# Kernel tuning notes

Hardware: AMD Instinct MI355X
Metric: run time of the kernel (lower is better)

Reference implementation:

```python
import jax, jax.numpy as jnp
import numpy as np

D_MODEL = 2048
D_STATE = 128
D_CONV = 4
NHEADS = 64
NGROUPS = 1
HEAD_DIM = 64
CHUNK = 128
EPS = 1e-5
D_INNER = NHEADS * HEAD_DIM                       # 4096
CONV_DIM = D_INNER + 2 * NGROUPS * D_STATE        # 4352
D_IN_PROJ = 2 * D_INNER + 2 * NGROUPS * D_STATE + NHEADS  # 8512


def setup_inputs() -> dict:
    key = jax.random.key(0)
    ks = jax.random.split(key, 9)
    B, S = 2, 4096
    return dict(
        hidden_states=jax.random.normal(ks[0], (B, S, D_MODEL), jnp.float32),
        W_in=jax.random.normal(ks[1], (D_MODEL, D_IN_PROJ), jnp.float32) * 0.02,
        conv_w=jax.random.normal(ks[2], (CONV_DIM, D_CONV), jnp.float32) * 0.2,
        conv_b=jax.random.normal(ks[3], (CONV_DIM,), jnp.float32) * 0.1,
        # A must be negative (stable SSM): A = -exp(u), u ~ U[0,2)
        A=-jnp.exp(jax.random.uniform(ks[4], (NHEADS,), jnp.float32, 0.0, 2.0)),
        D=jax.random.normal(ks[5], (NHEADS,), jnp.float32),
        dt_bias=jax.random.normal(ks[6], (NHEADS,), jnp.float32),
        norm_w=jnp.ones((D_INNER,), jnp.float32),
        W_out=jax.random.normal(ks[7], (D_INNER, D_MODEL), jnp.float32) * 0.02,
    )


def _silu(x):
    return x * jax.nn.sigmoid(x)


def _causal_conv1d(x, w, b):
    # depthwise causal conv with silu; x [B,S,C], w [C,K], b [C]
    K = w.shape[1]
    S = x.shape[1]
    xp = jnp.pad(x, ((0, 0), (K - 1, 0), (0, 0)))
    y = sum(xp[:, k:k + S, :] * w[None, None, :, k].swapaxes(-1, -1) for k in range(0))
    y = jnp.zeros_like(x)
    for k in range(K):
        y = y + xp[:, k:k + S, :] * w[:, k][None, None, :]
    return _silu(y + b)


def _ssd(x, dt, A, Bm, Cm, chunk):
    # Mamba2 chunked SSD scan.
    # x [b,s,h,p]; dt [b,s,h] (>0); A [h]; Bm,Cm [b,s,g,n]
    b, s, h, p = x.shape
    g, n = Bm.shape[2], Bm.shape[3]
    hh = h // g
    c = s // chunk
    x = x.reshape(b, c, chunk, g, hh, p)
    dt = dt.reshape(b, c, chunk, g, hh)
    Bm = Bm.reshape(b, c, chunk, g, n)
    Cm = Cm.reshape(b, c, chunk, g, n)
    dA = dt * A.reshape(g, hh)                 # [b,c,l,g,hh]
    dA_cs = jnp.cumsum(dA, axis=2)             # [b,c,l,g,hh]
    dtx = dt[..., None] * x                    # [b,c,l,g,hh,p]
    # intra-chunk (diagonal blocks): L[i,j] = exp(sum_{j<k<=i} dA)
    diff = dA_cs[:, :, :, None] - dA_cs[:, :, None, :]   # [b,c,i,j,g,hh]
    mask = jnp.tril(jnp.ones((chunk, chunk), bool))
    L = jnp.exp(jnp.where(mask[None, None, :, :, None, None], diff, -jnp.inf))
    Y = jnp.einsum('bcign,bcjgn,bcijgh,bcjghp->bcighp', Cm, Bm, L, dtx)
    # chunk-final states
    decay = jnp.exp(dA_cs[:, :, -1:] - dA_cs)            # [b,c,l,g,hh]
    states = jnp.einsum('bcjgn,bcjgh,bcjghp->bcghpn', Bm, decay, dtx)
    chunk_decay = jnp.exp(dA_cs[:, :, -1])               # [b,c,g,hh]
    def step(prev, inp):
        cd, st = inp
        return cd[..., None, None] * prev + st, prev
    init = jnp.zeros_like(states[:, 0])
    _, prevs = jax.lax.scan(step, init,
                            (jnp.moveaxis(chunk_decay, 1, 0), jnp.moveaxis(states, 1, 0)))
    prevs = jnp.moveaxis(prevs, 0, 1)                    # [b,c,g,hh,p,n] state entering each chunk
    Y = Y + jnp.einsum('bcign,bcghpn,bcigh->bcighp', Cm, prevs, jnp.exp(dA_cs))
    return Y.reshape(b, s, h, p)


def reference(hidden_states, W_in, conv_w, conv_b, A, D, dt_bias, norm_w, W_out):
    Bsz, S, _ = hidden_states.shape
    zxbcdt = hidden_states @ W_in                        # [B,S,d_in_proj]
    z = zxbcdt[..., :D_INNER]
    xbc = zxbcdt[..., D_INNER:D_INNER + CONV_DIM]
    dt = zxbcdt[..., D_INNER + CONV_DIM:]                # [B,S,nheads]
    xbc = _causal_conv1d(xbc, conv_w, conv_b)            # silu-activated causal conv
    x = xbc[..., :D_INNER].reshape(Bsz, S, NHEADS, HEAD_DIM)
    Bm = xbc[..., D_INNER:D_INNER + NGROUPS * D_STATE].reshape(Bsz, S, NGROUPS, D_STATE)
    Cm = xbc[..., D_INNER + NGROUPS * D_STATE:].reshape(Bsz, S, NGROUPS, D_STATE)
    dt = jax.nn.softplus(dt + dt_bias)                   # delta_softplus, dt_limit=(0,inf)
    y = _ssd(x, dt, A, Bm, Cm, CHUNK)
    y = y + D[None, None, :, None] * x                   # skip (D) term
    y = y.reshape(Bsz, S, D_INNER)
    # gated RMSNorm (norm_before_gate=False): normalize(y * silu(z)), grouped
    yg = y * _silu(z)
    gsz = D_INNER // NGROUPS
    ygr = yg.reshape(Bsz, S, NGROUPS, gsz)
    rms = jax.lax.rsqrt(jnp.mean(ygr * ygr, axis=-1, keepdims=True) + EPS)
    yn = (ygr * rms).reshape(Bsz, S, D_INNER) * norm_w
    return yn @ W_out
```

## Files before the change

### kernel.cpp

```cpp
#include <hip/hip_runtime.h>
#include <hip/hip_bf16.h>

typedef __bf16 bf16_t;
typedef bf16_t bf16x8 __attribute__((ext_vector_type(8)));
typedef float f32x4 __attribute__((ext_vector_type(4)));

#define TOK 8192
#define DMODEL 2048
#define DINNER 4096
#define XBCN 4352
#define DSTATE 128
#define NH 64
#define HD 64
#define NBC 64
#define WINT_ROWS 8448

__device__ __forceinline__ void gld16(const bf16_t* g, bf16_t* l) {
  __builtin_amdgcn_global_load_lds((const __attribute__((address_space(1))) void*)g,
                                   (__attribute__((address_space(3))) void*)l, 16, 0, 0);
}

__device__ __forceinline__ f32x4 mfma16(bf16x8 a, bf16x8 b, f32x4 c) {
  return __builtin_amdgcn_mfma_f32_16x16x32_bf16(a, b, c, 0, 0, 0);
}

__device__ __forceinline__ bf16x8 ldsr(unsigned addr) {
  f32x4 r;
  asm volatile("ds_read_b128 %0, %1" : "=v"(r) : "v"(addr));
  return __builtin_bit_cast(bf16x8, r);
}


__global__ __launch_bounds__(256)
void cast_split_kernel(const float* __restrict__ in, bf16_t* __restrict__ hi,
                       bf16_t* __restrict__ lo, size_t n) {
  size_t i = ((size_t)blockIdx.x * 256 + threadIdx.x) * 8;
  if (i + 8 > n) return;
  float4 a = *(const float4*)(in + i);
  float4 b = *(const float4*)(in + i + 4);
  float v[8] = {a.x,a.y,a.z,a.w,b.x,b.y,b.z,b.w};
  bf16x8 h, l;
#pragma unroll
  for (int j = 0; j < 8; ++j) {
    h[j] = (bf16_t)v[j];
    l[j] = (bf16_t)(v[j] - (float)h[j]);
  }
  *(bf16x8*)(hi + i) = h;
  *(bf16x8*)(lo + i) = l;
}

__global__ __launch_bounds__(256)
void transpose_cast_kernel(const float* __restrict__ in, bf16_t* __restrict__ out,
                           int R, int C, int outRows) {
  __shared__ float tile[32][33];
  const int c0 = blockIdx.x * 32;
  const int r0 = blockIdx.y * 32;
  const int tx = threadIdx.x & 31;
  const int ty = threadIdx.x >> 5;
#pragma unroll
  for (int k = 0; k < 4; ++k) {
    int r = r0 + ty + k*8;
    int c = c0 + tx;
    tile[ty + k*8][tx] = (c < C) ? in[(size_t)r * C + c] : 0.f;
  }
  __syncthreads();
#pragma unroll
  for (int k = 0; k < 4; ++k) {
    int oc = c0 + ty + k*8;
    int orr = r0 + tx;
    out[(size_t)oc * R + orr] = (bf16_t)tile[tx][ty + k*8];
  }
}

__global__ __launch_bounds__(256)
void wdt_split_kernel(const float* __restrict__ Win, bf16_t* __restrict__ Whi,
                      bf16_t* __restrict__ Wlo) {
  const int h = threadIdx.x & 63;
  const int k0 = blockIdx.x * 256 + (threadIdx.x >> 6) * 64;
#pragma unroll 4
  for (int i = 0; i < 64; ++i) {
    int k = k0 + i;
    float v = Win[(size_t)k * 8512 + 8448 + h];
    bf16_t hv = (bf16_t)v;
    Whi[(size_t)h * DMODEL + k] = hv;
    Wlo[(size_t)h * DMODEL + k] = (bf16_t)(v - (float)hv);
  }
}

template <typename OutT>
__global__ __launch_bounds__(512, 2)
void gemm256(const bf16_t* __restrict__ A, const bf16_t* __restrict__ B,
             OutT* __restrict__ C0, OutT* __restrict__ C1,
             long M, long N, long K, long splitN, int gridX) {
  __shared__ bf16_t sA[2][2][8192];
  __shared__ bf16_t sB[2][2][8192];
  const int tid = threadIdx.x;
  const int lane = tid & 63;
  const int wid = tid >> 6;
  const int wr = wid >> 2;
  const int wc = wid & 3;

  const int x = blockIdx.x & 7;
  const int q = blockIdx.x >> 3;
  const long bm = (long)(x * 4 + (q & 3)) * 256;
  const long bn = (long)(q >> 2) * 256;

  const int srow = (wid >> 1) * 16 + (lane & 15);
  const int skof = (wid & 1) * 32 + (lane >> 4) * 8;
  const bf16_t* Abase = A + (bm + srow) * K + skof;
  const bf16_t* Bbase = B + (bn + srow) * K + skof;

  auto stageA = [&](int buf, int h, long kt) {
    const bf16_t* s = Abase + (long)h * 128 * K + kt;
    gld16(s,          &sA[buf][h][wid * 512]);
    gld16(s + 64 * K, &sA[buf][h][4096 + wid * 512]);
  };
  auto stageB = [&](int buf, int h, long kt) {
    const bf16_t* s = Bbase + (long)h * 128 * K + kt;
    gld16(s,          &sB[buf][h][wid * 512]);
    gld16(s + 64 * K, &sB[buf][h][4096 + wid * 512]);
  };

  const unsigned sAb = (unsigned)(uintptr_t)(__attribute__((address_space(3))) void*)&sA[0][0][0]
                       + (unsigned)lane * 16 + (unsigned)wr * 8192;
  const unsigned sBb = (unsigned)(uintptr_t)(__attribute__((address_space(3))) void*)&sB[0][0][0]
                       + (unsigned)lane * 16 + (unsigned)wc * 4096;

  stageA(0, 0, 0); stageB(0, 0, 0); stageB(0, 1, 0); stageA(0, 1, 0);

  f32x4 acc[8][4] = {};
  bf16x8 a0[4][2], a1[4][2], b0[2][2], b1[2][2];
  int cur = 0;
  const int NT = (int)(K >> 6);

  for (int t = 0; t < NT; ++t) {
    const bool fin = (t == NT - 1);
    const long ktn = (long)(t + 1) * 64;
    const unsigned ab = sAb + (unsigned)cur * 32768;
    const unsigned bb = sBb + (unsigned)cur * 32768;

    asm volatile("s_waitcnt vmcnt(0)\n\ts_barrier" ::: "memory");

#pragma unroll
    for (int mi = 0; mi < 4; ++mi) {
      a0[mi][0] = ldsr(ab + (mi*2+0)*1024);
      a0[mi][1] = ldsr(ab + (mi*2+1)*1024);
    }
#pragma unroll
    for (int ni = 0; ni < 2; ++ni) {
      b0[ni][0] = ldsr(bb + (ni*2+0)*1024);
      b0[ni][1] = ldsr(bb + (ni*2+1)*1024);
    }
    if (!fin) { stageA(cur ^ 1, 0, ktn); stageB(cur ^ 1, 0, ktn); }
    asm volatile("s_waitcnt lgkmcnt(0)" ::: "memory");
    __builtin_amdgcn_sched_barrier(0);

#pragma unroll
    for (int ni = 0; ni < 2; ++ni) {
      b1[ni][0] = ldsr(bb + 16384 + (ni*2+0)*1024);
      b1[ni][1] = ldsr(bb + 16384 + (ni*2+1)*1024);
    }
    if (!fin) stageB(cur ^ 1, 1, ktn);
    __builtin_amdgcn_sched_barrier(0);
    __builtin_amdgcn_s_setprio(1);
#pragma unroll
    for (int mi = 0; mi < 4; ++mi)
#pragma unroll
      for (int ni = 0; ni < 2; ++ni) {
        acc[mi][ni] = mfma16(a0[mi][0], b0[ni][0], acc[mi][ni]);
        acc[mi][ni] = mfma16(a0[mi][1], b0[ni][1], acc[mi][ni]);
      }
    __builtin_amdgcn_s_setprio(0);
    __builtin_amdgcn_sched_barrier(0);
    asm volatile("s_waitcnt lgkmcnt(0)" ::: "memory");
    __builtin_amdgcn_sched_barrier(0);

#pragma unroll
    for (int mi = 0; mi < 4; ++mi) {
      a1[mi][0] = ldsr(ab + 16384 + (mi*2+0)*1024);
      a1[mi][1] = ldsr(ab + 16384 + (mi*2+1)*1024);
    }
    if (!fin) stageA(cur ^ 1, 1, ktn);
    __builtin_amdgcn_sched_barrier(0);
    __builtin_amdgcn_s_setprio(1);
#pragma unroll
    for (int mi = 0; mi < 4; ++mi)
#pragma unroll
      for (int ni = 0; ni < 2; ++ni) {
        acc[mi][2 + ni] = mfma16(a0[mi][0], b1[ni][0], acc[mi][2 + ni]);
        acc[mi][2 + ni] = mfma16(a0[mi][1], b1[ni][1], acc[mi][2 + ni]);
      }
    __builtin_amdgcn_s_setprio(0);
    __builtin_amdgcn_sched_barrier(0);
    asm volatile("s_waitcnt lgkmcnt(0)" ::: "memory");
    __builtin_amdgcn_sched_barrier(0);

    __builtin_amdgcn_s_setprio(1);
#pragma unroll
    for (int mi = 0; mi < 4; ++mi)
#pragma unroll
      for (int ni = 0; ni < 2; ++ni) {
        acc[4 + mi][2 + ni] = mfma16(a1[mi][0], b1[ni][0], acc[4 + mi][2 + ni]);
        acc[4 + mi][2 + ni] = mfma16(a1[mi][1], b1[ni][1], acc[4 + mi][2 + ni]);
      }
#pragma unroll
    for (int mi = 0; mi < 4; ++mi)
#pragma unroll
      for (int ni = 0; ni < 2; ++ni) {
        acc[4 + mi][ni] = mfma16(a1[mi][0], b0[ni][0], acc[4 + mi][ni]);
        acc[4 + mi][ni] = mfma16(a1[mi][1], b0[ni][1], acc[4 + mi][ni]);
      }
    __builtin_amdgcn_s_setprio(0);
    __builtin_amdgcn_sched_barrier(0);
    cur ^= 1;
  }

  const int cr = (lane >> 4) * 4;
  const int cc = lane & 15;
  OutT* Cb;
  long col0, ldc;
  if (bn < splitN) { Cb = C0; col0 = bn; ldc = splitN; }
  else             { Cb = C1; col0 = bn - splitN; ldc = N - splitN; }
#pragma unroll
  for (int mi = 0; mi < 8; ++mi) {
    long row = bm + (mi >> 2) * 128 + wr * 64 + (mi & 3) * 16 + cr;
#pragma unroll
    for (int ni = 0; ni < 4; ++ni) {
      long col = col0 + (ni >> 1) * 128 + wc * 32 + (ni & 1) * 16 + cc;
      OutT* p = Cb + row * ldc + col;
#pragma unroll
      for (int r = 0; r < 4; ++r) p[(long)r * ldc] = (OutT)acc[mi][ni][r];
    }
  }
}

__global__ __launch_bounds__(256)
void dt_mfma_kernel(const bf16_t* __restrict__ Ahi, const bf16_t* __restrict__ Alo,
                    const bf16_t* __restrict__ Whi, const bf16_t* __restrict__ Wlo,
                    float* __restrict__ dtraw) {
  __shared__ bf16_t sAh[4096], sAl[4096], sBh[2048], sBl[2048];
  const int tid = threadIdx.x;
  const int lane = tid & 63;
  const int w = tid >> 6;
  const long bm = (long)blockIdx.x * 128;
  const int rlo = lane & 15;
  const int kq = lane >> 4;

  const bf16_t* Ah0 = Ahi + (bm + 2*w*16 + rlo) * (long)DMODEL + kq*8;
  const bf16_t* Ah1 = Ah0 + 16*(long)DMODEL;
  const bf16_t* Al0 = Alo + (bm + 2*w*16 + rlo) * (long)DMODEL + kq*8;
  const bf16_t* Al1 = Al0 + 16*(long)DMODEL;
  const bf16_t* Bh0 = Whi + (w*16 + rlo) * (long)DMODEL + kq*8;
  const bf16_t* Bl0 = Wlo + (w*16 + rlo) * (long)DMODEL + kq*8;

  f32x4 acc[2][4] = {};

  for (int kt = 0; kt < DMODEL; kt += 32) {
    __syncthreads();
    gld16(Ah0 + kt, &sAh[(2*w)*512]);
    gld16(Ah1 + kt, &sAh[(2*w+1)*512]);
    gld16(Al0 + kt, &sAl[(2*w)*512]);
    gld16(Al1 + kt, &sAl[(2*w+1)*512]);
    gld16(Bh0 + kt, &sBh[w*512]);
    gld16(Bl0 + kt, &sBl[w*512]);
    __syncthreads();
    bf16x8 ah[2], al[2], bh[4], bl[4];
#pragma unroll
    for (int i = 0; i < 2; ++i) {
      ah[i] = *(const bf16x8*)&sAh[((2*w + i)*64 + lane)*8];
      al[i] = *(const bf16x8*)&sAl[((2*w + i)*64 + lane)*8];
    }
#pragma unroll
    for (int n = 0; n < 4; ++n) {
      bh[n] = *(const bf16x8*)&sBh[(n*64 + lane)*8];
      bl[n] = *(const bf16x8*)&sBl[(n*64 + lane)*8];
    }
#pragma unroll
    for (int mi = 0; mi < 2; ++mi)
#pragma unroll
      for (int n = 0; n < 4; ++n) {
        acc[mi][n] = mfma16(ah[mi], bh[n], acc[mi][n]);
        acc[mi][n] = mfma16(ah[mi], bl[n], acc[mi][n]);
        acc[mi][n] = mfma16(al[mi], bh[n], acc[mi][n]);
      }
  }

  const int cr = (lane >> 4) * 4;
  const int cc = lane & 15;
#pragma unroll
  for (int mi = 0; mi < 2; ++mi)
#pragma unroll
    for (int n = 0; n < 4; ++n)
#pragma unroll
      for (int r = 0; r < 4; ++r)
        dtraw[(bm + 2*w*16 + mi*16 + cr + r) * 64 + n*16 + cc] = acc[mi][n][r];
}

__global__ __launch_bounds__(256)
void conv_kernel(const bf16_t* __restrict__ xbc, const float* __restrict__ cw,
                 const float* __restrict__ cb, bf16_t* __restrict__ xo,
                 bf16_t* __restrict__ Bout, bf16_t* __restrict__ Cout) {
  const int c = blockIdx.x * 256 + threadIdx.x;
  const int t0 = blockIdx.y * 8;
  const int bstart = (t0 >> 12) << 12;
  const float w0 = cw[c*4+0], w1 = cw[c*4+1], w2 = cw[c*4+2], w3 = cw[c*4+3];
  const float bias = cb[c];
  float in[11];
#pragma unroll
  for (int k = 0; k < 11; ++k) {
    int t = t0 - 3 + k;
    in[k] = (t >= bstart) ? (float)xbc[(size_t)t * XBCN + c] : 0.f;
  }
#pragma unroll
  for (int i = 0; i < 8; ++i) {
    float v = bias + w0*in[i] + w1*in[i+1] + w2*in[i+2] + w3*in[i+3];
    float s = v / (1.f + __expf(-v));
    int t = t0 + i;
    bf16_t o = (bf16_t)s;
    if (c < DINNER)           xo[(size_t)t * DINNER + c] = o;
    else if (c < DINNER+128)  Bout[(size_t)t * DSTATE + (c - DINNER)] = o;
    else                      Cout[(size_t)t * DSTATE + (c - DINNER - 128)] = o;
  }
}

__global__ __launch_bounds__(256)
void dt_scan_kernel(const float* __restrict__ dtraw, const float* __restrict__ dt_bias,
                    const float* __restrict__ Avec, float* __restrict__ dt_s,
                    float* __restrict__ dAcs, float* __restrict__ cdec) {
  const int wid = blockIdx.x * 4 + (threadIdx.x >> 6);
  const int lane = threadIdx.x & 63;
  const int h = wid & 63;
  const int bc = wid >> 6;
  const long tok0 = (long)bc * 128;
  const float Ah = Avec[h];
  const float bias = dt_bias[h];
  float v0 = dtraw[(tok0 + lane)*64 + h] + bias;
  float v1 = dtraw[(tok0 + 64 + lane)*64 + h] + bias;
  float d0 = (v0 > 20.f) ? v0 : log1pf(expf(v0));
  float d1 = (v1 > 20.f) ? v1 : log1pf(expf(v1));
  float s0 = d0 * Ah;
  float s1 = d1 * Ah;
#pragma unroll
  for (int off = 1; off < 64; off <<= 1) {
    float t = __shfl_up(s0, off);
    if (lane >= off) s0 += t;
  }
  float tot0 = __shfl(s0, 63);
#pragma unroll
  for (int off = 1; off < 64; off <<= 1) {
    float t = __shfl_up(s1, off);
    if (lane >= off) s1 += t;
  }
  s1 += tot0;
  const size_t base = (size_t)wid * 128;
  dt_s[base + lane] = d0;
  dt_s[base + 64 + lane] = d1;
  dAcs[base + lane] = s0;
  dAcs[base + 64 + lane] = s1;
  if (lane == 63) cdec[wid] = __expf(s1);
}

__global__ __launch_bounds__(256)
void states_kernel(const bf16_t* __restrict__ x, const bf16_t* __restrict__ Bm,
                   const float* __restrict__ dt_s, const float* __restrict__ dAcs,
                   bf16_t* __restrict__ states) {
  __shared__ bf16_t sDtx[8192];
  __shared__ bf16_t sBd[16384];
  __shared__ float sDt[128];
  __shared__ float sDec[128];
  const int wid = blockIdx.x;
  const int h = wid & 63;
  const int bc = wid >> 6;
  const int tid = threadIdx.x;
  const int lane = tid & 63;
  const int w = tid >> 6;
  const long tok0 = (long)bc * 128;
  const size_t dbase = (size_t)wid * 128;

  if (tid < 128) {
    sDt[tid] = dt_s[dbase + tid];
  } else {
    int j = tid - 128;
    sDec[j] = __expf(dAcs[dbase + 127] - dAcs[dbase + j]);
  }
  __syncthreads();

  {
    const int jj0 = tid >> 3;
    const int pg = (tid & 7) * 8;
#pragma unroll
    for (int t = 0; t < 4; ++t) {
      int j = t*32 + jj0;
      bf16x8 xv = *(const bf16x8*)&x[(tok0 + j)*(long)DINNER + h*64 + pg];
      float dtj = sDt[j];
      int kq = (j >> 5) * 4;
      int qe = ((j >> 3) & 3) * 16;
      int e = j & 7;
#pragma unroll
      for (int i = 0; i < 8; ++i) {
        int p = pg + i;
        sDtx[((kq + (p>>4))*64 + qe + (p&15))*8 + e] = (bf16_t)((float)xv[i]*dtj);
      }
    }
    const int jj1 = tid >> 4;
    const int ng = (tid & 15) * 8;
#pragma unroll
    for (int t = 0; t < 8; ++t) {
      int j = t*16 + jj1;
      bf16x8 bv = *(const bf16x8*)&Bm[(tok0 + j)*(long)DSTATE + ng];
      float dec = sDec[j];
      int kq = (j >> 5) * 8;
      int qe = ((j >> 3) & 3) * 16;
      int e = j & 7;
#pragma unroll
      for (int i = 0; i < 8; ++i) {
        int n = ng + i;
        sBd[((kq + (n>>4))*64 + qe + (n&15))*8 + e] = (bf16_t)((float)bv[i]*dec);
      }
    }
  }
  __syncthreads();

  f32x4 acc[4][2] = {};
#pragma unroll
  for (int kt = 0; kt < 4; ++kt) {
    bf16x8 aF[4], bF[2];
#pragma unroll
    for (int mt = 0; mt < 4; ++mt) aF[mt] = *(const bf16x8*)&sDtx[((kt*4 + mt)*64 + lane)*8];
#pragma unroll
    for (int nt = 0; nt < 2; ++nt) bF[nt] = *(const bf16x8*)&sBd[((kt*8 + w*2 + nt)*64 + lane)*8];
#pragma unroll
    for (int mt = 0; mt < 4; ++mt)
#pragma unroll
      for (int nt = 0; nt < 2; ++nt)
        acc[mt][nt] = mfma16(aF[mt], bF[nt], acc[mt][nt]);
  }

  bf16_t* S = states + (size_t)wid * (HD * DSTATE);
  const int cr = (lane >> 4) * 4;
  const int cc = lane & 15;
#pragma unroll
  for (int mt = 0; mt < 4; ++mt)
#pragma unroll
    for (int nt = 0; nt < 2; ++nt) {
      int n = (w*2 + nt)*16 + cc;
#pragma unroll
      for (int r = 0; r < 4; ++r) {
        int p = mt*16 + cr + r;
        S[(size_t)p*DSTATE + n] = (bf16_t)acc[mt][nt][r];
      }
    }
}

__global__ __launch_bounds__(256)
void scan_kernel(bf16_t* __restrict__ sp, const float* __restrict__ cdec) {
  const size_t gid = (size_t)blockIdx.x * 256 + threadIdx.x;
  const int n = gid & 127;
  const int p = (gid >> 7) & 63;
  const int h = (gid >> 13) & 63;
  const int b = (int)(gid >> 19);
  float prev = 0.f;
  const size_t pn = (size_t)p * 128 + n;
  for (int c = 0; c < 32; ++c) {
    const int wid = (b*32 + c)*64 + h;
    const size_t idx = (size_t)wid * 8192 + pn;
    float s = (float)sp[idx];
    sp[idx] = (bf16_t)prev;
    prev = cdec[wid] * prev + s;
  }
}

__global__ __launch_bounds__(256)
void ssd_y_kernel(bf16_t* __restrict__ xy, const bf16_t* __restrict__ Bm,
                  const bf16_t* __restrict__ Cm, const bf16_t* __restrict__ prevs,
                  const float* __restrict__ dt_s, const float* __restrict__ dAcs,
                  const float* __restrict__ Dvec) {
  __shared__ bf16_t sG[16384];
  __shared__ bf16_t sDtx[8192];
  __shared__ float sDA[128];
  __shared__ float sEA[128];
  __shared__ float sDt[128];

  const int wid = blockIdx.x;
  const int h = wid & 63;
  const int bc = wid >> 6;
  const int tid = threadIdx.x;
  const int lane = tid & 63;
  const int w = tid >> 6;
  const long tok0 = (long)bc * 128;
  const size_t dbase = (size_t)wid * 128;

  if (tid < 128) {
    float v = dAcs[dbase + tid];
    sDA[tid] = v;
    sEA[tid] = __expf(v);
  } else {
    sDt[tid - 128] = dt_s[dbase + tid - 128];
  }
  __syncthreads();

  {
    const int jj0 = tid >> 3;
    const int pg = (tid & 7) * 8;
#pragma unroll
    for (int t = 0; t < 4; ++t) {
      int j = t*32 + jj0;
      bf16x8 xv = *(const bf16x8*)&xy[(tok0 + j)*(long)DINNER + h*64 + pg];
      float dtj = sDt[j];
      int kq = (j >> 5) * 4;
      int qe = ((j >> 3) & 3) * 16;
      int e = j & 7;
#pragma unroll
      for (int i = 0; i < 8; ++i) {
        int p = pg + i;
        sDtx[((kq + (p>>4))*64 + qe + (p&15))*8 + e] = (bf16_t)((float)xv[i]*dtj);
      }
    }
  }

  const int arow = (w*2)*16 + (lane & 15);
  const int koff = (lane >> 4) * 8;
  bf16x8 aCm[2][4];
#pragma unroll
  for (int mi = 0; mi < 2; ++mi)
#pragma unroll
    for (int kt = 0; kt < 4; ++kt)
      aCm[mi][kt] = *(const bf16x8*)&Cm[(tok0 + arow + mi*16)*(long)DSTATE + kt*32 + koff];

  const bf16_t* P = prevs + (size_t)wid * 8192;
  f32x4 accY[2][4] = {};
#pragma unroll
  for (int kt = 0; kt < 4; ++kt) {
    bf16x8 bP[4];
#pragma unroll
    for (int ni = 0; ni < 4; ++ni)
      bP[ni] = *(const bf16x8*)&P[(size_t)(ni*16 + (lane & 15))*DSTATE + kt*32 + koff];
#pragma unroll
    for (int mi = 0; mi < 2; ++mi)
#pragma unroll
      for (int ni = 0; ni < 4; ++ni)
        accY[mi][ni] = mfma16(aCm[mi][kt], bP[ni], accY[mi][ni]);
  }
  const int cr = (lane >> 4) * 4;
  const int cc = lane & 15;
#pragma unroll
  for (int mi = 0; mi < 2; ++mi)
#pragma unroll
    for (int r = 0; r < 4; ++r) {
      float e = sEA[(w*2 + mi)*16 + cr + r];
#pragma unroll
      for (int ni = 0; ni < 4; ++ni) accY[mi][ni][r] *= e;
    }

  f32x4 accS[2][8] = {};
#pragma unroll
  for (int kt = 0; kt < 4; ++kt) {
    bf16x8 bB[8];
#pragma unroll
    for (int nt = 0; nt < 8; ++nt)
      bB[nt] = *(const bf16x8*)&Bm[(tok0 + nt*16 + (lane & 15))*(long)DSTATE + kt*32 + koff];
#pragma unroll
    for (int mi = 0; mi < 2; ++mi)
#pragma unroll
      for (int nt = 0; nt < 8; ++nt)
        accS[mi][nt] = mfma16(aCm[mi][kt], bB[nt], accS[mi][nt]);
  }

#pragma unroll
  for (int mi = 0; mi < 2; ++mi)
#pragma unroll
    for (int nt = 0; nt < 8; ++nt)
#pragma unroll
      for (int r = 0; r < 4; ++r) {
        int i = (w*2 + mi)*16 + cr + r;
        int j = nt*16 + cc;
        float g = (i >= j) ? accS[mi][nt][r] * __expf(sDA[i] - sDA[j]) : 0.f;
        sG[(((j>>5)*8 + (i>>4))*64 + ((j>>3)&3)*16 + (i&15))*8 + (j&7)] = (bf16_t)g;
      }
  __syncthreads();

#pragma unroll
  for (int kt = 0; kt < 4; ++kt) {
    bf16x8 aG[2], bD[4];
#pragma unroll
    for (int mi = 0; mi < 2; ++mi) aG[mi] = *(const bf16x8*)&sG[((kt*8 + w*2 + mi)*64 + lane)*8];
#pragma unroll
    for (int ni = 0; ni < 4; ++ni) bD[ni] = *(const bf16x8*)&sDtx[((kt*4 + ni)*64 + lane)*8];
#pragma unroll
    for (int mi = 0; mi < 2; ++mi)
#pragma unroll
      for (int ni = 0; ni < 4; ++ni)
        accY[mi][ni] = mfma16(aG[mi], bD[ni], accY[mi][ni]);
  }

  const float Dh = Dvec[h];
#pragma unroll
  for (int mi = 0; mi < 2; ++mi)
#pragma unroll
    for (int ni = 0; ni < 4; ++ni)
#pragma unroll
      for (int r = 0; r < 4; ++r) {
        long tokr = tok0 + (w*2 + mi)*16 + cr + r;
        int p = ni*16 + cc;
        long idx = tokr * DINNER + h*64 + p;
        float xv = (float)xy[idx];
        xy[idx] = (bf16_t)(accY[mi][ni][r] + Dh * xv);
      }
}

__global__ __launch_bounds__(256)
void gate_kernel(const bf16_t* __restrict__ y, const bf16_t* __restrict__ z,
                 const float* __restrict__ norm_w, bf16_t* __restrict__ yn) {
  const int tok = blockIdx.x;
  const int tid = threadIdx.x;
  const int lane = tid & 63;
  const int w = tid >> 6;
  const bf16_t* yrow = y + (size_t)tok * DINNER;
  const bf16_t* zrow = z + (size_t)tok * DINNER;
  float local[16];
  float ss = 0.f;
#pragma unroll
  for (int v = 0; v < 2; ++v) {
    int col = tid*16 + v*8;
    bf16x8 yv = *(const bf16x8*)&yrow[col];
    bf16x8 zv = *(const bf16x8*)&zrow[col];
#pragma unroll
    for (int i = 0; i < 8; ++i) {
      float zf = (float)zv[i];
      float g = zf / (1.f + __expf(-zf));
      float t = (float)yv[i] * g;
      local[v*8 + i] = t;
      ss += t*t;
    }
  }
#pragma unroll
  for (int off = 32; off > 0; off >>= 1) ss += __shfl_xor(ss, off);
  __shared__ float red[4];
  if (lane == 0) red[w] = ss;
  __syncthreads();
  float rms = rsqrtf((red[0]+red[1]+red[2]+red[3]) * (1.f/DINNER) + 1e-5f);
  bf16_t* orow = yn + (size_t)tok * DINNER;
#pragma unroll
  for (int v = 0; v < 2; ++v) {
    int col = tid*16 + v*8;
    bf16x8 o;
#pragma unroll
    for (int i = 0; i < 8; ++i) o[i] = (bf16_t)(local[v*8+i] * rms * norm_w[col+i]);
    *(bf16x8*)&orow[col] = o;
  }
}

extern "C" void kernel_launch(void* const* d_in, const int* in_sizes, int n_in,
                              void* d_out, int out_size, void* d_ws, size_t ws_size,
                              hipStream_t stream) {
  const float* hidden  = (const float*)d_in[0];
  const float* W_in    = (const float*)d_in[1];
  const float* conv_w  = (const float*)d_in[2];
  const float* conv_b  = (const float*)d_in[3];
  const float* Avec    = (const float*)d_in[4];
  const float* Dvec    = (const float*)d_in[5];
  const float* dt_bias = (const float*)d_in[6];
  const float* norm_w  = (const float*)d_in[7];
  const float* W_out   = (const float*)d_in[8];

  char* ws = (char*)d_ws;
  size_t off = 0;
  auto take = [&](size_t bytes) -> char* {
    char* p = ws + off;
    off += (bytes + 255) & ~(size_t)255;
    return p;
  };
  bf16_t* R1    = (bf16_t*)take((size_t)NBC * NH * HD * DSTATE * 2);
  bf16_t* WinT  = (bf16_t*)take((size_t)WINT_ROWS * DMODEL * 2);
  bf16_t* xbc   = (bf16_t*)take((size_t)TOK * XBCN * 2);
  bf16_t* xconv = (bf16_t*)take((size_t)TOK * DINNER * 2);
  bf16_t* Bmat  = (bf16_t*)take((size_t)TOK * DSTATE * 2);
  bf16_t* Cmat  = (bf16_t*)take((size_t)TOK * DSTATE * 2);
  float*  dtraw = (float*)take((size_t)TOK * NH * 4);
  float*  dt_s  = (float*)take((size_t)TOK * NH * 4);
  float*  dAcs  = (float*)take((size_t)TOK * NH * 4);
  float*  cdec  = (float*)take((size_t)NBC * NH * 4);
  bf16_t* Wdth  = (bf16_t*)take((size_t)NH * DMODEL * 2);
  bf16_t* Wdtl  = (bf16_t*)take((size_t)NH * DMODEL * 2);
  if (off > ws_size) return;

  bf16_t* Xb      = R1;
  bf16_t* Xlo     = xbc;
  bf16_t* statesB = R1;
  bf16_t* ynbuf   = R1;
  bf16_t* WoutT   = WinT;
  bf16_t* zbuf    = (bf16_t*)d_out;
  float*  out     = (float*)d_out;

  cast_split_kernel<<<(TOK*DMODEL)/2048, 256, 0, stream>>>(hidden, Xb, Xlo, (size_t)TOK*DMODEL);
  wdt_split_kernel<<<DMODEL/256, 256, 0, stream>>>(W_in, Wdth, Wdtl);
  dt_mfma_kernel<<<TOK/128, 256, 0, stream>>>(Xb, Xlo, Wdth, Wdtl, dtraw);
  transpose_cast_kernel<<<dim3(WINT_ROWS/32, DMODEL/32), 256, 0, stream>>>(W_in, WinT, DMODEL, 8512, WINT_ROWS);
  gemm256<bf16_t><<<(TOK/256)*(WINT_ROWS/256), 512, 0, stream>>>(
      Xb, WinT, zbuf, xbc, TOK, WINT_ROWS, DMODEL, DINNER, WINT_ROWS/256);
  transpose_cast_kernel<<<dim3(DMODEL/32, DINNER/32), 256, 0, stream>>>(W_out, WoutT, DINNER, DMODEL, DMODEL);
  conv_kernel<<<dim3(XBCN/256, TOK/8), 256, 0, stream>>>(xbc, conv_w, conv_b, xconv, Bmat, Cmat);
  dt_scan_kernel<<<(NBC*NH)/4, 256, 0, stream>>>(dtraw, dt_bias, Avec, dt_s, dAcs, cdec);
  states_kernel<<<NBC*NH, 256, 0, stream>>>(xconv, Bmat, dt_s, dAcs, statesB);
  scan_kernel<<<(NBC*NH*HD*DSTATE)/(32*256), 256, 0, stream>>>(statesB, cdec);
  ssd_y_kernel<<<NBC*NH, 256, 0, stream>>>(xconv, Bmat, Cmat, statesB, dt_s, dAcs, Dvec);
  gate_kernel<<<TOK, 256, 0, stream>>>(xconv, zbuf, norm_w, ynbuf);
  gemm256<float><<<(TOK/256)*(DMODEL/256), 512, 0, stream>>>(
      ynbuf, WoutT, out, out, TOK, DMODEL, DINNER, DMODEL, DMODEL/256);
}
```

Before: 1.053 ms.

## Restructure GEMM main loop into 8-phase ping-pong pipeline with partial vmcnt waits

Rewrites the 256x256 bf16 GEMM k-loop to process two k-tiles per iteration in eight phases. Each phase issues LDS reads and one quarter-tile global-to-LDS prefetch, then runs an MFMA quadrant between barriers. It prefetches deeper, with the next buffer staged up front, and waits on vmcnt(6) instead of vmcnt(0), so global loads stay in flight across the MFMA phases. The cost is more s_barrier calls per tile and tighter ordering assumptions on buffer reuse, which could cause races if a stage overwrites data still being read.

```diff
diff --git a/kernel.cpp b/kernel.cpp
--- a/kernel.cpp
+++ b/kernel.cpp
@@ -86,6 +86,51 @@
     Wlo[(size_t)h * DMODEL + k] = (bf16_t)(v - (float)hv);
   }
 }
+
+#define PH_MID() \
+  __builtin_amdgcn_sched_barrier(0); \
+  asm volatile("s_barrier" ::: "memory"); \
+  asm volatile("s_waitcnt lgkmcnt(0)" ::: "memory"); \
+  __builtin_amdgcn_sched_barrier(0); \
+  __builtin_amdgcn_s_setprio(1)
+
+#define PH_END() \
+  __builtin_amdgcn_s_setprio(0); \
+  __builtin_amdgcn_sched_barrier(0); \
+  asm volatile("s_barrier" ::: "memory")
+
+#define PH_END_VM6() \
+  __builtin_amdgcn_s_setprio(0); \
+  __builtin_amdgcn_sched_barrier(0); \
+  asm volatile("s_waitcnt vmcnt(6)\n\ts_barrier" ::: "memory")
+
+#define PH_END_VM0() \
+  __builtin_amdgcn_s_setprio(0); \
+  __builtin_amdgcn_sched_barrier(0); \
+  asm volatile("s_waitcnt vmcnt(0)\n\ts_barrier" ::: "memory")
+
+#define RD_A(arr, base) \
+  _Pragma("unroll") \
+  for (int mi = 0; mi < 4; ++mi) { \
+    arr[mi][0] = ldsr((base) + (mi*2+0)*1024); \
+    arr[mi][1] = ldsr((base) + (mi*2+1)*1024); \
+  }
+
+#define RD_B(arr, base) \
+  _Pragma("unroll") \
+  for (int ni = 0; ni < 2; ++ni) { \
+    arr[ni][0] = ldsr((base) + (ni*2+0)*1024); \
+    arr[ni][1] = ldsr((base) + (ni*2+1)*1024); \
+  }
+
+#define MMAQ(MB, NB, aa, bb2) \
+  _Pragma("unroll") \
+  for (int mi = 0; mi < 4; ++mi) \
+    _Pragma("unroll") \
+    for (int ni = 0; ni < 2; ++ni) { \
+      acc[(MB)+mi][(NB)+ni] = mfma16(aa[mi][0], bb2[ni][0], acc[(MB)+mi][(NB)+ni]); \
+      acc[(MB)+mi][(NB)+ni] = mfma16(aa[mi][1], bb2[ni][1], acc[(MB)+mi][(NB)+ni]); \
+    }
 
 template <typename OutT>
 __global__ __launch_bounds__(512, 2)
@@ -121,98 +166,81 @@
     gld16(s + 64 * K, &sB[buf][h][4096 + wid * 512]);
   };
 
-  const unsigned sAb = (unsigned)(uintptr_t)(__attribute__((address_space(3))) void*)&sA[0][0][0]
-                       + (unsigned)lane * 16 + (unsigned)wr * 8192;
-  const unsigned sBb = (unsigned)(uintptr_t)(__attribute__((address_space(3))) void*)&sB[0][0][0]
-                       + (unsigned)lane * 16 + (unsigned)wc * 4096;
+  const unsigned ldsA = (unsigned)(uintptr_t)(__attribute__((address_space(3))) void*)&sA[0][0][0]
+                        + (unsigned)lane * 16 + (unsigned)wr * 8192;
+  const unsigned ldsB = (unsigned)(uintptr_t)(__attribute__((address_space(3))) void*)&sB[0][0][0]
+                        + (unsigned)lane * 16 + (unsigned)wc * 4096;
+  const unsigned ab0 = ldsA;
+  const unsigned ab0h = ldsA + 16384;
+  const unsigned ab1 = ldsA + 32768;
+  const unsigned ab1h = ldsA + 49152;
+  const unsigned bb0 = ldsB;
+  const unsigned bb0h = ldsB + 16384;
+  const unsigned bb1 = ldsB + 32768;
+  const unsigned bb1h = ldsB + 49152;
 
   stageA(0, 0, 0); stageB(0, 0, 0); stageB(0, 1, 0); stageA(0, 1, 0);
+  stageA(1, 0, 64); stageB(1, 0, 64); stageB(1, 1, 64);
+  __builtin_amdgcn_sched_barrier(0);
+  asm volatile("s_waitcnt vmcnt(6)\n\ts_barrier" ::: "memory");
 
   f32x4 acc[8][4] = {};
   bf16x8 a0[4][2], a1[4][2], b0[2][2], b1[2][2];
-  int cur = 0;
-  const int NT = (int)(K >> 6);
-
-  for (int t = 0; t < NT; ++t) {
-    const bool fin = (t == NT - 1);
-    const long ktn = (long)(t + 1) * 64;
-    const unsigned ab = sAb + (unsigned)cur * 32768;
-    const unsigned bb = sBb + (unsigned)cur * 32768;
-
-    asm volatile("s_waitcnt vmcnt(0)\n\ts_barrier" ::: "memory");
-
-#pragma unroll
-    for (int mi = 0; mi < 4; ++mi) {
-      a0[mi][0] = ldsr(ab + (mi*2+0)*1024);
-      a0[mi][1] = ldsr(ab + (mi*2+1)*1024);
-    }
-#pragma unroll
-    for (int ni = 0; ni < 2; ++ni) {
-      b0[ni][0] = ldsr(bb + (ni*2+0)*1024);
-      b0[ni][1] = ldsr(bb + (ni*2+1)*1024);
-    }
-    if (!fin) { stageA(cur ^ 1, 0, ktn); stageB(cur ^ 1, 0, ktn); }
-    asm volatile("s_waitcnt lgkmcnt(0)" ::: "memory");
-    __builtin_amdgcn_sched_barrier(0);
-
-#pragma unroll
-    for (int ni = 0; ni < 2; ++ni) {
-      b1[ni][0] = ldsr(bb + 16384 + (ni*2+0)*1024);
-      b1[ni][1] = ldsr(bb + 16384 + (ni*2+1)*1024);
-    }
-    if (!fin) stageB(cur ^ 1, 1, ktn);
-    __builtin_amdgcn_sched_barrier(0);
-    __builtin_amdgcn_s_setprio(1);
-#pragma unroll
-    for (int mi = 0; mi < 4; ++mi)
-#pragma unroll
-      for (int ni = 0; ni < 2; ++ni) {
-        acc[mi][ni] = mfma16(a0[mi][0], b0[ni][0], acc[mi][ni]);
-        acc[mi][ni] = mfma16(a0[mi][1], b0[ni][1], acc[mi][ni]);
-      }
-    __builtin_amdgcn_s_setprio(0);
-    __builtin_amdgcn_sched_barrier(0);
-    asm volatile("s_waitcnt lgkmcnt(0)" ::: "memory");
-    __builtin_amdgcn_sched_barrier(0);
-
-#pragma unroll
-    for (int mi = 0; mi < 4; ++mi) {
-      a1[mi][0] = ldsr(ab + 16384 + (mi*2+0)*1024);
-      a1[mi][1] = ldsr(ab + 16384 + (mi*2+1)*1024);
-    }
-    if (!fin) stageA(cur ^ 1, 1, ktn);
-    __builtin_amdgcn_sched_barrier(0);
-    __builtin_amdgcn_s_setprio(1);
-#pragma unroll
-    for (int mi = 0; mi < 4; ++mi)
-#pragma unroll
-      for (int ni = 0; ni < 2; ++ni) {
-        acc[mi][2 + ni] = mfma16(a0[mi][0], b1[ni][0], acc[mi][2 + ni]);
-        acc[mi][2 + ni] = mfma16(a0[mi][1], b1[ni][1], acc[mi][2 + ni]);
-      }
-    __builtin_amdgcn_s_setprio(0);
-    __builtin_amdgcn_sched_barrier(0);
-    asm volatile("s_waitcnt lgkmcnt(0)" ::: "memory");
-    __builtin_amdgcn_sched_barrier(0);
-
-    __builtin_amdgcn_s_setprio(1);
-#pragma unroll
-    for (int mi = 0; mi < 4; ++mi)
-#pragma unroll
-      for (int ni = 0; ni < 2; ++ni) {
-        acc[4 + mi][2 + ni] = mfma16(a1[mi][0], b1[ni][0], acc[4 + mi][2 + ni]);
-        acc[4 + mi][2 + ni] = mfma16(a1[mi][1], b1[ni][1], acc[4 + mi][2 + ni]);
-      }
-#pragma unroll
-    for (int mi = 0; mi < 4; ++mi)
-#pragma unroll
-      for (int ni = 0; ni < 2; ++ni) {
-        acc[4 + mi][ni] = mfma16(a1[mi][0], b0[ni][0], acc[4 + mi][ni]);
-        acc[4 + mi][ni] = mfma16(a1[mi][1], b0[ni][1], acc[4 + mi][ni]);
-      }
-    __builtin_amdgcn_s_setprio(0);
-    __builtin_amdgcn_sched_barrier(0);
-    cur ^= 1;
+  const int NI = (int)(K >> 7);
+
+  for (int i = 0; i < NI; ++i) {
+    const bool fin = (i == NI - 1);
+    const long k1 = ((long)(2*i + 1)) << 6;
+    const long k2 = k1 + 64;
+    const long k3 = k1 + 128;
+
+    RD_A(a0, ab0);
+    RD_B(b0, bb0);
+    stageA(1, 1, k1);
+    PH_MID();
+    MMAQ(0, 0, a0, b0);
+    PH_END();
+
+    RD_B(b1, bb0h);
+    if (!fin) stageA(0, 0, k2);
+    PH_MID();
+    MMAQ(0, 2, a0, b1);
+    PH_END();
+
+    RD_A(a1, ab0h);
+    if (!fin) stageB(0, 0, k2);
+    PH_MID();
+    MMAQ(4, 2, a1, b1);
+    PH_END();
+
+    if (!fin) stageB(0, 1, k2);
+    PH_MID();
+    MMAQ(4, 0, a1, b0);
+    if (!fin) { PH_END_VM6(); } else { PH_END_VM0(); }
+
+    RD_A(a0, ab1);
+    RD_B(b0, bb1);
+    if (!fin) stageA(0, 1, k2);
+    PH_MID();
+    MMAQ(0, 0, a0, b0);
+    PH_END();
+
+    RD_B(b1, bb1h);
+    if (!fin) stageA(1, 0, k3);
+    PH_MID();
+    MMAQ(0, 2, a0, b1);
+    PH_END();
+
+    RD_A(a1, ab1h);
+    if (!fin) stageB(1, 0, k3);
+    PH_MID();
+    MMAQ(4, 2, a1, b1);
+    PH_END();
+
+    if (!fin) stageB(1, 1, k3);
+    PH_MID();
+    MMAQ(4, 0, a1, b0);
+    if (!fin) { PH_END_VM6(); } else { PH_END(); }
   }
 
   const int cr = (lane >> 4) * 4;
```

Measured after the change: 996.6 us. 5.4% less time.
